# Kernel optimization log

Hardware: AMD Instinct MI355X
Metric: run time of the kernel (lower is better)

## Reference

```python
import jax, jax.numpy as jnp
import numpy as np

D_MODEL = 1024
N_HEADS = 16
D_K = D_MODEL // N_HEADS


def setup_inputs() -> dict:
    key = jax.random.key(0)
    ks = jax.random.split(key, 9)
    s = 1.0 / np.sqrt(D_MODEL)
    inp = {
        'x': jax.random.normal(ks[0], (2, 2048, D_MODEL), dtype=jnp.float32),
        'wq': jax.random.normal(ks[1], (D_MODEL, D_MODEL), dtype=jnp.float32) * s,
        'bq': jnp.zeros((D_MODEL,), dtype=jnp.float32),
        'wk': jax.random.normal(ks[2], (D_MODEL, D_MODEL), dtype=jnp.float32) * s,
        'bk': jnp.zeros((D_MODEL,), dtype=jnp.float32),
        'wv': jax.random.normal(ks[3], (D_MODEL, D_MODEL), dtype=jnp.float32) * s,
        'bv': jnp.zeros((D_MODEL,), dtype=jnp.float32),
        'wo': jax.random.normal(ks[4], (D_MODEL, D_MODEL), dtype=jnp.float32) * s,
        'bo': jnp.zeros((D_MODEL,), dtype=jnp.float32),
    }
    return inp


def _rope_tables(seq_len, dim, dtype):
    inv_freq = 1.0 / (10000.0 ** (jnp.arange(0, dim, 2, dtype=jnp.float32) / dim))
    t = jnp.arange(seq_len, dtype=jnp.float32)
    freqs = jnp.einsum('i,j->ij', t, inv_freq)          # [S, dim/2]
    emb = jnp.concatenate([freqs, freqs], axis=-1)       # [S, dim]
    return jnp.cos(emb).astype(dtype), jnp.sin(emb).astype(dtype)


def _rotate_half(x):
    half = x.shape[-1] // 2
    return jnp.concatenate([-x[..., half:], x[..., :half]], axis=-1)


def reference(x, wq, bq, wk, bk, wv, bv, wo, bo):
    B, S, _ = x.shape
    H, Dk = N_HEADS, D_K
    # QKV projections (torch Linear: x @ W^T + b)
    q = (x @ wq.T + bq).reshape(B, S, H, Dk).transpose(0, 2, 1, 3)  # [B,H,S,Dk]
    k = (x @ wk.T + bk).reshape(B, S, H, Dk).transpose(0, 2, 1, 3)
    v = (x @ wv.T + bv).reshape(B, S, H, Dk).transpose(0, 2, 1, 3)
    # RoPE
    cos, sin = _rope_tables(S, Dk, x.dtype)  # [S, Dk] each
    q = q * cos + _rotate_half(q) * sin
    k = k * cos + _rotate_half(k) * sin
    # scaled dot-product attention (full scores, softmax over keys)
    scores = jnp.einsum('bhqd,bhkd->bhqk', q, k) / jnp.sqrt(jnp.asarray(Dk, x.dtype))
    attn = jax.nn.softmax(scores, axis=-1)
    out = jnp.einsum('bhqk,bhkd->bqhd', attn, v).reshape(B, S, H * Dk)
    return out @ wo.T + bo
```

## Files before the change

### kernel.cpp

```cpp
#include <hip/hip_runtime.h>
#include <stdint.h>


typedef __attribute__((ext_vector_type(8))) __bf16 bf16x8;
typedef __attribute__((ext_vector_type(4))) __bf16 bf16x4;
typedef __attribute__((ext_vector_type(4))) short short4v;
typedef __attribute__((ext_vector_type(4))) unsigned short ushort4v;
typedef __attribute__((ext_vector_type(4))) float f32x4;

#define GLDS(gp, lp)                                                          \
  __builtin_amdgcn_global_load_lds(                                           \
      (const __attribute__((address_space(1))) void*)(gp),                    \
      (__attribute__((address_space(3))) void*)(lp), 16, 0, 0)

__device__ __forceinline__ unsigned short f2bf(float f) {
  unsigned u = __float_as_uint(f);
  return (unsigned short)((u + 0x7fffu + ((u >> 16) & 1u)) >> 16);
}
__device__ __forceinline__ float bf2f(unsigned short b) {
  return __uint_as_float(((unsigned)b) << 16);
}

__global__ __launch_bounds__(256) void cvt_all_k(
    const float* __restrict__ x, const float* __restrict__ wq,
    const float* __restrict__ wk, const float* __restrict__ wv,
    const float* __restrict__ wo, unsigned short* __restrict__ xb,
    unsigned short* __restrict__ wqb, unsigned short* __restrict__ wkb,
    unsigned short* __restrict__ wvb, unsigned short* __restrict__ wob) {
  const long i = (long)(blockIdx.x * 256 + threadIdx.x) * 4;
  const float* src;
  unsigned short* dst;
  long off;
  if (i < 4194304L) {
    src = x; dst = xb; off = i;
  } else {
    long j = i - 4194304L;
    int w = (int)(j >> 20);
    off = j & 1048575L;
    src = (w == 0) ? wq : (w == 1) ? wk : (w == 2) ? wv : wo;
    dst = (w == 0) ? wqb : (w == 1) ? wkb : (w == 2) ? wvb : wob;
  }
  f32x4 v = *(const f32x4*)(src + off);
  ushort4v o;
  o[0] = f2bf(v[0]); o[1] = f2bf(v[1]); o[2] = f2bf(v[2]); o[3] = f2bf(v[3]);
  *(ushort4v*)(dst + off) = o;
}

__global__ __launch_bounds__(256) void rope_tables_k(float* __restrict__ cosT,
                                                     float* __restrict__ sinT) {
  const int idx = blockIdx.x * 256 + threadIdx.x;
  const int s = idx >> 5, i = idx & 31;
  const float freq = (float)s * exp2f(-(float)i * (13.287712379549449f / 32.0f));
  cosT[idx] = cosf(freq);
  sinT[idx] = sinf(freq);
}

__device__ __forceinline__ void gemm_core(const unsigned short* __restrict__ A,
                                          const unsigned short* __restrict__ W,
                                          unsigned short* As, unsigned short* Bs,
                                          int rowBase, int colBase,
                                          f32x4 acc[4][4]) {
  const int lane = threadIdx.x & 63, wid = threadIdx.x >> 6;
  const int wr = wid >> 1, wc = wid & 1;
  const int lr = lane >> 3, l8 = lane & 7;
  const int swz = (l8 ^ lr) * 8;
  const int c16 = lane & 15, g = lane >> 4;

  const f32x4 zero = {0.f, 0.f, 0.f, 0.f};
#pragma unroll
  for (int mf = 0; mf < 4; ++mf)
#pragma unroll
    for (int nf = 0; nf < 4; ++nf) acc[mf][nf] = zero;

  for (int kt = 0; kt < 16; ++kt) {
    __syncthreads();
#pragma unroll
    for (int c2 = 0; c2 < 4; ++c2) {
      const int cc = wid * 4 + c2;
      const int r = cc * 8 + lr;
      GLDS(A + (size_t)(rowBase + r) * 1024 + kt * 64 + swz, As + cc * 512);
      GLDS(W + (size_t)(colBase + r) * 1024 + kt * 64 + swz, Bs + cc * 512);
    }
    __syncthreads();
#pragma unroll
    for (int ks = 0; ks < 2; ++ks) {
      bf16x8 af[4], bfr[4];
#pragma unroll
      for (int mf = 0; mf < 4; ++mf) {
        const int r = wr * 64 + mf * 16 + c16;
        const int kb = (g * 16 + ks * 64) ^ ((r & 7) * 16);
        af[mf] = *(const bf16x8*)((const char*)As + r * 128 + kb);
      }
#pragma unroll
      for (int nf = 0; nf < 4; ++nf) {
        const int r = wc * 64 + nf * 16 + c16;
        const int kb = (g * 16 + ks * 64) ^ ((r & 7) * 16);
        bfr[nf] = *(const bf16x8*)((const char*)Bs + r * 128 + kb);
      }
#pragma unroll
      for (int mf = 0; mf < 4; ++mf)
#pragma unroll
        for (int nf = 0; nf < 4; ++nf)
          acc[mf][nf] = __builtin_amdgcn_mfma_f32_16x16x32_bf16(
              af[mf], bfr[nf], acc[mf][nf], 0, 0, 0);
    }
  }
}

__global__ __launch_bounds__(256) void qkv_gemm_k(
    const unsigned short* __restrict__ xb, const unsigned short* __restrict__ wqb,
    const unsigned short* __restrict__ wkb, const unsigned short* __restrict__ wvb,
    const float* __restrict__ bq, const float* __restrict__ bk,
    const float* __restrict__ bv, unsigned short* __restrict__ Qp,
    unsigned short* __restrict__ Kp, unsigned short* __restrict__ Vt) {
  __shared__ unsigned short As[8192], Bs[8192];
  const int z = blockIdx.z;
  const unsigned short* W = (z == 0) ? wqb : (z == 1) ? wkb : wvb;
  const float* bias = (z == 0) ? bq : (z == 1) ? bk : bv;
  const int rowBase = blockIdx.x * 128, colBase = blockIdx.y * 128;
  f32x4 acc[4][4];
  gemm_core(xb, W, As, Bs, rowBase, colBase, acc);

  const int lane = threadIdx.x & 63, wid = threadIdx.x >> 6;
  const int wr = wid >> 1, wc = wid & 1, c16 = lane & 15, g = lane >> 4;
  if (z <= 1) {
    unsigned short* dst = z ? Kp : Qp;
#pragma unroll
    for (int nf = 0; nf < 4; ++nf) {
      const int col = colBase + wc * 64 + nf * 16 + c16;
      const float bb = bias[col];
#pragma unroll
      for (int mf = 0; mf < 4; ++mf) {
        const int r0 = rowBase + wr * 64 + mf * 16 + g * 4;
#pragma unroll
        for (int reg = 0; reg < 4; ++reg)
          dst[(size_t)(r0 + reg) * 1024 + col] = f2bf(acc[mf][nf][reg] + bb);
      }
    }
  } else {
#pragma unroll
    for (int nf = 0; nf < 4; ++nf) {
      const int col = colBase + wc * 64 + nf * 16 + c16;
      const float bb = bias[col];
#pragma unroll
      for (int mf = 0; mf < 4; ++mf) {
        const int n0 = rowBase + wr * 64 + mf * 16 + g * 4;
        const int btc = n0 >> 11, s0 = n0 & 2047;
        ushort4v pk;
#pragma unroll
        for (int reg = 0; reg < 4; ++reg) pk[reg] = f2bf(acc[mf][nf][reg] + bb);
        *(ushort4v*)(Vt + ((size_t)(btc * 1024 + col)) * 2048 + s0) = pk;
      }
    }
  }
}

__global__ __launch_bounds__(256) void out_gemm_k(
    const unsigned short* __restrict__ attn, const unsigned short* __restrict__ wob,
    const float* __restrict__ bo, float* __restrict__ out) {
  __shared__ unsigned short As[8192], Bs[8192];
  const int rowBase = blockIdx.x * 128, colBase = blockIdx.y * 128;
  f32x4 acc[4][4];
  gemm_core(attn, wob, As, Bs, rowBase, colBase, acc);

  const int lane = threadIdx.x & 63, wid = threadIdx.x >> 6;
  const int wr = wid >> 1, wc = wid & 1, c16 = lane & 15, g = lane >> 4;
#pragma unroll
  for (int nf = 0; nf < 4; ++nf) {
    const int col = colBase + wc * 64 + nf * 16 + c16;
    const float bb = bo[col];
#pragma unroll
    for (int mf = 0; mf < 4; ++mf) {
      const int r0 = rowBase + wr * 64 + mf * 16 + g * 4;
#pragma unroll
      for (int reg = 0; reg < 4; ++reg)
        out[(size_t)(r0 + reg) * 1024 + col] = acc[mf][nf][reg] + bb;
    }
  }
}

__global__ __launch_bounds__(256) void rope_apply_k(
    const unsigned short* __restrict__ Qp, const unsigned short* __restrict__ Kp,
    const float* __restrict__ cosT, const float* __restrict__ sinT,
    unsigned short* __restrict__ Qr, unsigned short* __restrict__ Kr) {
  const float SC = 0.125f * 1.44269504088896f;
  const int idx = blockIdx.x * 256 + threadIdx.x;
  const int i = idx & 31;
  const int s = (idx >> 5) & 2047;
  const int bh = idx >> 16;
  const int b = bh >> 4, h = bh & 15;
  const size_t src = (size_t)(b * 2048 + s) * 1024 + h * 64 + i;
  const float c = cosT[(s << 5) + i], sn = sinT[(s << 5) + i];
  const float q0 = bf2f(Qp[src]), q1 = bf2f(Qp[src + 32]);
  const float k0 = bf2f(Kp[src]), k1 = bf2f(Kp[src + 32]);
  const size_t d0 = (size_t)(bh * 2048 + s) * 64 + i;
  Qr[d0] = f2bf((q0 * c - q1 * sn) * SC);
  Qr[d0 + 32] = f2bf((q1 * c + q0 * sn) * SC);
  Kr[d0] = f2bf(k0 * c - k1 * sn);
  Kr[d0 + 32] = f2bf(k1 * c + k0 * sn);
}

__global__ __launch_bounds__(256) void attn_k(
    const unsigned short* __restrict__ Qr, const unsigned short* __restrict__ Kr,
    const unsigned short* __restrict__ Vt, unsigned short* __restrict__ attn) {
  __shared__ unsigned short Ks[3][4096], Vs[3][4096];
  const int lane = threadIdx.x & 63, w = threadIdx.x >> 6;
  const int qt = blockIdx.x, bh = blockIdx.y;
  const int c = lane & 15, g = lane >> 4;
  const int l3 = lane >> 3, l7 = lane & 7;
  const int swz8 = (l7 ^ l3) * 8;
  const unsigned short* Qh = Qr + (size_t)bh * 2048 * 64;
  const unsigned short* Kh = Kr + (size_t)bh * 2048 * 64;
  const unsigned short* Vh = Vt + (size_t)bh * 64 * 2048;
  const int qbase = qt * 128 + w * 32;

  const bf16x8 qa0 = *(const bf16x8*)(Qh + (size_t)(qbase + c) * 64 + g * 8);
  const bf16x8 qa1 =
      *(const bf16x8*)(Qh + (size_t)(qbase + c) * 64 + g * 8 + 32);
  const bf16x8 qb0 =
      *(const bf16x8*)(Qh + (size_t)(qbase + 16 + c) * 64 + g * 8);
  const bf16x8 qb1 =
      *(const bf16x8*)(Qh + (size_t)(qbase + 16 + c) * 64 + g * 8 + 32);

  f32x4 oa[4], ob[4];
#pragma unroll
  for (int b2 = 0; b2 < 4; ++b2) {
    oa[b2] = (f32x4){0.f, 0.f, 0.f, 0.f};
    ob[b2] = (f32x4){0.f, 0.f, 0.f, 0.f};
  }
  f32x4 oea = {0.f, 0.f, 0.f, 0.f}, oeb = oea;
  const short4v ones = {0x3F80, 0x3F80, 0x3F80, 0x3F80};
  const f32x4 cinit = {-12.f, -12.f, -12.f, -12.f};

#define STAGE(ktile, buf)                                                     \
  do {                                                                        \
    char* KsB_ = (char*)&Ks[buf][0];                                          \
    char* VsB_ = (char*)&Vs[buf][0];                                          \
    _Pragma("unroll") for (int j = 0; j < 4; ++j) {                           \
      const int ch = w * 4 + j;                                               \
      if (ch < 8) {                                                           \
        GLDS(Kh + (size_t)((ktile)*64 + ch * 8 + l3) * 64 + swz8,             \
             KsB_ + ch * 1024);                                               \
      } else {                                                                \
        const int cv = ch - 8;                                                \
        GLDS(Vh + (size_t)(cv * 8 + l3) * 2048 + (ktile)*64 + swz8,           \
             VsB_ + cv * 1024);                                               \
      }                                                                       \
    }                                                                         \
  } while (0)

  STAGE(0, 0);
  STAGE(1, 1);
  asm volatile("s_waitcnt vmcnt(4)" ::: "memory");
  __syncthreads();
  int bc = 0, bs = 2;

  for (int kt = 0; kt < 32; ++kt) {
    if (kt < 30) STAGE(kt + 2, bs);
    const char* KsB = (const char*)&Ks[bc][0];
    const char* VsB = (const char*)&Vs[bc][0];

    f32x4 sa[4], sb[4];
    __builtin_amdgcn_s_setprio(1);
#pragma unroll
    for (int kk = 0; kk < 4; ++kk) {
      const int r = kk * 16 + c;
      const bf16x8 kf0 =
          *(const bf16x8*)(KsB + r * 128 + ((g * 16) ^ ((c & 7) * 16)));
      const bf16x8 kf1 =
          *(const bf16x8*)(KsB + r * 128 + ((64 + g * 16) ^ ((c & 7) * 16)));
      f32x4 t = __builtin_amdgcn_mfma_f32_16x16x32_bf16(kf0, qa0, cinit, 0, 0, 0);
      sa[kk] = __builtin_amdgcn_mfma_f32_16x16x32_bf16(kf1, qa1, t, 0, 0, 0);
      f32x4 u = __builtin_amdgcn_mfma_f32_16x16x32_bf16(kf0, qb0, cinit, 0, 0, 0);
      sb[kk] = __builtin_amdgcn_mfma_f32_16x16x32_bf16(kf1, qb1, u, 0, 0, 0);
    }
    __builtin_amdgcn_s_setprio(0);

    short4v pba[4], pbb[4];
#pragma unroll
    for (int kk = 0; kk < 4; ++kk) {
      bf16x4 pa = {(__bf16)exp2f(sa[kk][0]), (__bf16)exp2f(sa[kk][1]),
                   (__bf16)exp2f(sa[kk][2]), (__bf16)exp2f(sa[kk][3])};
      bf16x4 pb = {(__bf16)exp2f(sb[kk][0]), (__bf16)exp2f(sb[kk][1]),
                   (__bf16)exp2f(sb[kk][2]), (__bf16)exp2f(sb[kk][3])};
      pba[kk] = __builtin_bit_cast(short4v, pa);
      pbb[kk] = __builtin_bit_cast(short4v, pb);
    }

    __builtin_amdgcn_s_setprio(1);
#pragma unroll
    for (int kk = 0; kk < 4; ++kk) {
#pragma unroll
      for (int b2 = 0; b2 < 4; ++b2) {
        const int vd = b2 * 16 + c;
        const short4v vf = *(const short4v*)(
            VsB + vd * 128 + ((kk * 32 + g * 8) ^ ((c & 7) * 16)));
        oa[b2] = __builtin_amdgcn_mfma_f32_16x16x16bf16_1k(vf, pba[kk], oa[b2],
                                                           0, 0, 0);
        ob[b2] = __builtin_amdgcn_mfma_f32_16x16x16bf16_1k(vf, pbb[kk], ob[b2],
                                                           0, 0, 0);
      }
      oea = __builtin_amdgcn_mfma_f32_16x16x16bf16_1k(ones, pba[kk], oea, 0, 0, 0);
      oeb = __builtin_amdgcn_mfma_f32_16x16x16bf16_1k(ones, pbb[kk], oeb, 0, 0, 0);
    }
    __builtin_amdgcn_s_setprio(0);

    if (kt < 31) {
      if (kt < 30) {
        asm volatile("s_waitcnt vmcnt(4)" ::: "memory");
      } else {
        asm volatile("s_waitcnt vmcnt(0)" ::: "memory");
      }
      __syncthreads();
    }
    bc = (bc == 2) ? 0 : bc + 1;
    bs = (bs == 2) ? 0 : bs + 1;
  }

  const float inva = 1.0f / oea[0];
  const float invb = 1.0f / oeb[0];
  const int b = bh >> 4, h = bh & 15;
  const int na = b * 2048 + qbase + c;
  unsigned short* opa = attn + (size_t)na * 1024 + h * 64;
  unsigned short* opb = opa + (size_t)16 * 1024;
#pragma unroll
  for (int b2 = 0; b2 < 4; ++b2) {
    ushort4v st;
    st[0] = f2bf(oa[b2][0] * inva);
    st[1] = f2bf(oa[b2][1] * inva);
    st[2] = f2bf(oa[b2][2] * inva);
    st[3] = f2bf(oa[b2][3] * inva);
    *(ushort4v*)(opa + b2 * 16 + g * 4) = st;
    ushort4v su;
    su[0] = f2bf(ob[b2][0] * invb);
    su[1] = f2bf(ob[b2][1] * invb);
    su[2] = f2bf(ob[b2][2] * invb);
    su[3] = f2bf(ob[b2][3] * invb);
    *(ushort4v*)(opb + b2 * 16 + g * 4) = su;
  }
}

extern "C" void kernel_launch(void* const* d_in, const int* in_sizes, int n_in,
                              void* d_out, int out_size, void* d_ws,
                              size_t ws_size, hipStream_t stream) {
  const float* x = (const float*)d_in[0];
  const float* wq = (const float*)d_in[1];
  const float* bq = (const float*)d_in[2];
  const float* wk = (const float*)d_in[3];
  const float* bk = (const float*)d_in[4];
  const float* wv = (const float*)d_in[5];
  const float* bv = (const float*)d_in[6];
  const float* wo = (const float*)d_in[7];
  const float* bo = (const float*)d_in[8];
  float* out = (float*)d_out;

  unsigned short* xb = (unsigned short*)d_ws;
  unsigned short* wqb = xb + 4194304;
  unsigned short* wkb = wqb + 1048576;
  unsigned short* wvb = wkb + 1048576;
  unsigned short* wob = wvb + 1048576;
  unsigned short* Qp = wob + 1048576;
  unsigned short* Kp = Qp + 4194304;
  unsigned short* Vt = Kp + 4194304;
  unsigned short* Kr = Vt + 4194304;
  float* cosT = (float*)(Kr + 4194304);
  float* sinT = cosT + 65536;
  unsigned short* Qr = xb;
  unsigned short* attn = Qp;

  cvt_all_k<<<dim3(8192), 256, 0, stream>>>(x, wq, wk, wv, wo, xb, wqb, wkb,
                                            wvb, wob);
  rope_tables_k<<<dim3(256), 256, 0, stream>>>(cosT, sinT);
  qkv_gemm_k<<<dim3(32, 8, 3), 256, 0, stream>>>(xb, wqb, wkb, wvb, bq, bk, bv,
                                                 Qp, Kp, Vt);
  rope_apply_k<<<dim3(8192), 256, 0, stream>>>(Qp, Kp, cosT, sinT, Qr, Kr);
  attn_k<<<dim3(16, 32), 256, 0, stream>>>(Qr, Kr, Vt, attn);
  out_gemm_k<<<dim3(32, 8), 256, 0, stream>>>(attn, wob, bo, out);
}
```

Before: 149.5 us.

## Fuse RoPE into QKV GEMM epilogue and use packed bf16 exp conversion

Applies the RoPE rotation and the Q scaling directly in the QKV GEMM epilogue and writes head-major Qr/Kr, so the separate rope_apply kernel and its full read/write round trip of Q and K are removed. The mapping relies on each wave's 64 columns being exactly one head, with rotation partners sitting in accumulator fragments nf and nf+2. Separately, the attention softmax now uses the hardware exp2 builtin and v_cvt_pk_bf16_f32 to pack probabilities two at a time. The fused epilogue does scattered 2-byte stores and extra cos/sin loads per row, which may cost some GEMM efficiency.

```diff
diff --git a/kernel.cpp b/kernel.cpp
--- a/kernel.cpp
+++ b/kernel.cpp
@@ -6,6 +6,7 @@
 typedef __attribute__((ext_vector_type(4))) __bf16 bf16x4;
 typedef __attribute__((ext_vector_type(4))) short short4v;
 typedef __attribute__((ext_vector_type(4))) unsigned short ushort4v;
+typedef __attribute__((ext_vector_type(2))) unsigned uint2v;
 typedef __attribute__((ext_vector_type(4))) float f32x4;
 
 #define GLDS(gp, lp)                                                          \
@@ -19,6 +20,13 @@
 }
 __device__ __forceinline__ float bf2f(unsigned short b) {
   return __uint_as_float(((unsigned)b) << 16);
+}
+__device__ __forceinline__ short4v cvtpk4(float a, float b, float c, float d) {
+  unsigned lo, hi;
+  asm("v_cvt_pk_bf16_f32 %0, %1, %2" : "=v"(lo) : "v"(a), "v"(b));
+  asm("v_cvt_pk_bf16_f32 %0, %1, %2" : "=v"(hi) : "v"(c), "v"(d));
+  uint2v u = {lo, hi};
+  return __builtin_bit_cast(short4v, u);
 }
 
 __global__ __launch_bounds__(256) void cvt_all_k(
@@ -111,8 +119,9 @@
     const unsigned short* __restrict__ xb, const unsigned short* __restrict__ wqb,
     const unsigned short* __restrict__ wkb, const unsigned short* __restrict__ wvb,
     const float* __restrict__ bq, const float* __restrict__ bk,
-    const float* __restrict__ bv, unsigned short* __restrict__ Qp,
-    unsigned short* __restrict__ Kp, unsigned short* __restrict__ Vt) {
+    const float* __restrict__ bv, const float* __restrict__ cosT,
+    const float* __restrict__ sinT, unsigned short* __restrict__ Qr,
+    unsigned short* __restrict__ Kr, unsigned short* __restrict__ Vt) {
   __shared__ unsigned short As[8192], Bs[8192];
   const int z = blockIdx.z;
   const unsigned short* W = (z == 0) ? wqb : (z == 1) ? wkb : wvb;
@@ -124,17 +133,33 @@
   const int lane = threadIdx.x & 63, wid = threadIdx.x >> 6;
   const int wr = wid >> 1, wc = wid & 1, c16 = lane & 15, g = lane >> 4;
   if (z <= 1) {
-    unsigned short* dst = z ? Kp : Qp;
-#pragma unroll
-    for (int nf = 0; nf < 4; ++nf) {
-      const int col = colBase + wc * 64 + nf * 16 + c16;
-      const float bb = bias[col];
-#pragma unroll
-      for (int mf = 0; mf < 4; ++mf) {
-        const int r0 = rowBase + wr * 64 + mf * 16 + g * 4;
-#pragma unroll
-        for (int reg = 0; reg < 4; ++reg)
-          dst[(size_t)(r0 + reg) * 1024 + col] = f2bf(acc[mf][nf][reg] + bb);
+    unsigned short* dst = z ? Kr : Qr;
+    const float SC = z ? 1.0f : 0.125f * 1.44269504088896f;
+    const int h = blockIdx.y * 2 + wc;
+    const float bb0 = bias[colBase + wc * 64 + 0 * 16 + c16];
+    const float bb1 = bias[colBase + wc * 64 + 1 * 16 + c16];
+    const float bb2 = bias[colBase + wc * 64 + 2 * 16 + c16];
+    const float bb3 = bias[colBase + wc * 64 + 3 * 16 + c16];
+#pragma unroll
+    for (int mf = 0; mf < 4; ++mf) {
+      const int n0 = rowBase + wr * 64 + mf * 16 + g * 4;
+#pragma unroll
+      for (int reg = 0; reg < 4; ++reg) {
+        const int n = n0 + reg;
+        const int b = n >> 11, s = n & 2047;
+        const float c0 = cosT[(s << 5) + c16], s0 = sinT[(s << 5) + c16];
+        const float c1 = cosT[(s << 5) + c16 + 16],
+                    s1 = sinT[(s << 5) + c16 + 16];
+        const float a0 = acc[mf][0][reg] + bb0;
+        const float a1 = acc[mf][1][reg] + bb1;
+        const float a2 = acc[mf][2][reg] + bb2;
+        const float a3 = acc[mf][3][reg] + bb3;
+        unsigned short* dp =
+            dst + (size_t)((b * 16 + h) * 2048 + s) * 64 + c16;
+        dp[0] = f2bf((a0 * c0 - a2 * s0) * SC);
+        dp[16] = f2bf((a1 * c1 - a3 * s1) * SC);
+        dp[32] = f2bf((a2 * c0 + a0 * s0) * SC);
+        dp[48] = f2bf((a3 * c1 + a1 * s1) * SC);
       }
     }
   } else {
@@ -177,27 +202,6 @@
         out[(size_t)(r0 + reg) * 1024 + col] = acc[mf][nf][reg] + bb;
     }
   }
-}
-
-__global__ __launch_bounds__(256) void rope_apply_k(
-    const unsigned short* __restrict__ Qp, const unsigned short* __restrict__ Kp,
-    const float* __restrict__ cosT, const float* __restrict__ sinT,
-    unsigned short* __restrict__ Qr, unsigned short* __restrict__ Kr) {
-  const float SC = 0.125f * 1.44269504088896f;
-  const int idx = blockIdx.x * 256 + threadIdx.x;
-  const int i = idx & 31;
-  const int s = (idx >> 5) & 2047;
-  const int bh = idx >> 16;
-  const int b = bh >> 4, h = bh & 15;
-  const size_t src = (size_t)(b * 2048 + s) * 1024 + h * 64 + i;
-  const float c = cosT[(s << 5) + i], sn = sinT[(s << 5) + i];
-  const float q0 = bf2f(Qp[src]), q1 = bf2f(Qp[src + 32]);
-  const float k0 = bf2f(Kp[src]), k1 = bf2f(Kp[src + 32]);
-  const size_t d0 = (size_t)(bh * 2048 + s) * 64 + i;
-  Qr[d0] = f2bf((q0 * c - q1 * sn) * SC);
-  Qr[d0 + 32] = f2bf((q1 * c + q0 * sn) * SC);
-  Kr[d0] = f2bf(k0 * c - k1 * sn);
-  Kr[d0 + 32] = f2bf(k1 * c + k0 * sn);
 }
 
 __global__ __launch_bounds__(256) void attn_k(
@@ -279,12 +283,14 @@
     short4v pba[4], pbb[4];
 #pragma unroll
     for (int kk = 0; kk < 4; ++kk) {
-      bf16x4 pa = {(__bf16)exp2f(sa[kk][0]), (__bf16)exp2f(sa[kk][1]),
-                   (__bf16)exp2f(sa[kk][2]), (__bf16)exp2f(sa[kk][3])};
-      bf16x4 pb = {(__bf16)exp2f(sb[kk][0]), (__bf16)exp2f(sb[kk][1]),
-                   (__bf16)exp2f(sb[kk][2]), (__bf16)exp2f(sb[kk][3])};
-      pba[kk] = __builtin_bit_cast(short4v, pa);
-      pbb[kk] = __builtin_bit_cast(short4v, pb);
+      pba[kk] = cvtpk4(__builtin_amdgcn_exp2f(sa[kk][0]),
+                       __builtin_amdgcn_exp2f(sa[kk][1]),
+                       __builtin_amdgcn_exp2f(sa[kk][2]),
+                       __builtin_amdgcn_exp2f(sa[kk][3]));
+      pbb[kk] = cvtpk4(__builtin_amdgcn_exp2f(sb[kk][0]),
+                       __builtin_amdgcn_exp2f(sb[kk][1]),
+                       __builtin_amdgcn_exp2f(sb[kk][2]),
+                       __builtin_amdgcn_exp2f(sb[kk][3]));
     }
 
     __builtin_amdgcn_s_setprio(1);
@@ -359,21 +365,18 @@
   unsigned short* wkb = wqb + 1048576;
   unsigned short* wvb = wkb + 1048576;
   unsigned short* wob = wvb + 1048576;
-  unsigned short* Qp = wob + 1048576;
-  unsigned short* Kp = Qp + 4194304;
-  unsigned short* Vt = Kp + 4194304;
-  unsigned short* Kr = Vt + 4194304;
-  float* cosT = (float*)(Kr + 4194304);
+  unsigned short* Qr = wob + 1048576;
+  unsigned short* Kr = Qr + 4194304;
+  unsigned short* Vt = Kr + 4194304;
+  unsigned short* attnb = Vt + 4194304;
+  float* cosT = (float*)(attnb + 4194304);
   float* sinT = cosT + 65536;
-  unsigned short* Qr = xb;
-  unsigned short* attn = Qp;
 
   cvt_all_k<<<dim3(8192), 256, 0, stream>>>(x, wq, wk, wv, wo, xb, wqb, wkb,
                                             wvb, wob);
   rope_tables_k<<<dim3(256), 256, 0, stream>>>(cosT, sinT);
   qkv_gemm_k<<<dim3(32, 8, 3), 256, 0, stream>>>(xb, wqb, wkb, wvb, bq, bk, bv,
-                                                 Qp, Kp, Vt);
-  rope_apply_k<<<dim3(8192), 256, 0, stream>>>(Qp, Kp, cosT, sinT, Qr, Kr);
-  attn_k<<<dim3(16, 32), 256, 0, stream>>>(Qr, Kr, Vt, attn);
-  out_gemm_k<<<dim3(32, 8), 256, 0, stream>>>(attn, wob, bo, out);
-}
+                                                 cosT, sinT, Qr, Kr, Vt);
+  attn_k<<<dim3(16, 32), 256, 0, stream>>>(Qr, Kr, Vt, attnb);
+  out_gemm_k<<<dim3(32, 8), 256, 0, stream>>>(attnb, wob, bo, out);
+}
```

Result: faster. 129.5 us (-13.4%).
